# Optimization experiments

Hardware: AMD Instinct MI355X
Metric: run time of the kernel (lower is better)

## Reference

```python
import jax, jax.numpy as jnp
import numpy as np

N_NODES = 10000
N_EDGES = 640000
D = 128  # node / edge / hidden feature dim
EPS = 1e-6


def _relu_mlp(x, params):
    # Dense+relu for all layers except the last (plain Dense)
    for w, b in params[:-1]:
        x = jax.nn.relu(x @ w + b)
    w, b = params[-1]
    return x @ w + b


def _layer_norm(x, scale, bias):
    mean = jnp.mean(x, axis=-1, keepdims=True)
    var = jnp.mean(jnp.square(x - mean), axis=-1, keepdims=True)
    return (x - mean) * jax.lax.rsqrt(var + EPS) * scale + bias


def _he(key, fan_in, fan_out):
    return jax.random.normal(key, (fan_in, fan_out), jnp.float32) * jnp.sqrt(2.0 / fan_in)


def setup_inputs() -> dict:
    key = jax.random.key(0)
    ks = jax.random.split(key, 12)
    nodes = jax.random.normal(ks[0], (N_NODES, D), jnp.float32)
    edges = jax.random.normal(ks[1], (N_EDGES, D), jnp.float32)
    senders = jax.random.randint(ks[2], (N_EDGES,), 0, N_NODES, jnp.int32)
    receivers = jax.random.randint(ks[3], (N_EDGES,), 0, N_NODES, jnp.int32)
    # MessageMLP: [3D -> D -> D -> D]
    msg_w0 = _he(ks[4], 3 * D, D); msg_b0 = jnp.zeros((D,), jnp.float32)
    msg_w1 = _he(ks[5], D, D);     msg_b1 = jnp.zeros((D,), jnp.float32)
    msg_w2 = _he(ks[6], D, D);     msg_b2 = jnp.zeros((D,), jnp.float32)
    # NodeMLP: [2D -> D -> D -> D]
    node_w0 = _he(ks[7], 2 * D, D); node_b0 = jnp.zeros((D,), jnp.float32)
    node_w1 = _he(ks[8], D, D);     node_b1 = jnp.zeros((D,), jnp.float32)
    node_w2 = _he(ks[9], D, D);     node_b2 = jnp.zeros((D,), jnp.float32)
    # W_node residual projection (no bias) + LayerNorm params
    w_node = _he(ks[10], D, D)
    ln_scale = jnp.ones((D,), jnp.float32)
    ln_bias = jnp.zeros((D,), jnp.float32)
    return dict(nodes=nodes, edges=edges, senders=senders, receivers=receivers,
                msg_w0=msg_w0, msg_b0=msg_b0, msg_w1=msg_w1, msg_b1=msg_b1,
                msg_w2=msg_w2, msg_b2=msg_b2,
                node_w0=node_w0, node_b0=node_b0, node_w1=node_w1, node_b1=node_b1,
                node_w2=node_w2, node_b2=node_b2,
                w_node=w_node, ln_scale=ln_scale, ln_bias=ln_bias)


def reference(nodes, edges, senders, receivers,
              msg_w0, msg_b0, msg_w1, msg_b1, msg_w2, msg_b2,
              node_w0, node_b0, node_w1, node_b1, node_w2, node_b2,
              w_node, ln_scale, ln_bias):
    total_nodes = nodes.shape[0]
    # gather sender/receiver features and concat with edge features: [E, 3D]
    msg_in = jnp.concatenate([nodes[senders], nodes[receivers], edges], axis=-1)
    messages = _relu_mlp(msg_in, [(msg_w0, msg_b0), (msg_w1, msg_b1), (msg_w2, msg_b2)])
    # scatter-add messages onto receiving nodes: [N, D]
    aggregated = jax.ops.segment_sum(messages, receivers, num_segments=total_nodes)
    node_in = jnp.concatenate([nodes, aggregated], axis=-1)  # [N, 2D]
    nodes_out = _relu_mlp(node_in, [(node_w0, node_b0), (node_w1, node_b1), (node_w2, node_b2)])
    nodes_new = _layer_norm(nodes @ w_node + nodes_out, ln_scale, ln_bias)
    return nodes_new
```

## Files before the change

kernel.cpp:

```cpp
#include <hip/hip_runtime.h>

#define DF 128
constexpr int N_NODES = 10000;
constexpr int N_EDGES = 640000;

typedef __bf16 bf16x8 __attribute__((ext_vector_type(8)));
typedef float f32x4 __attribute__((ext_vector_type(4)));

__device__ __forceinline__ unsigned short f2bf(float f) {
  unsigned u = __builtin_bit_cast(unsigned, f);
  u += 0x7fffu + ((u >> 16) & 1u);
  return (unsigned short)(u >> 16);
}

__device__ __forceinline__ bf16x8 cvt8(float4 a, float4 b) {
  bf16x8 r;
  r[0] = (__bf16)a.x; r[1] = (__bf16)a.y; r[2] = (__bf16)a.z; r[3] = (__bf16)a.w;
  r[4] = (__bf16)b.x; r[5] = (__bf16)b.y; r[6] = (__bf16)b.z; r[7] = (__bf16)b.w;
  return r;
}

template <bool RELU>
__device__ __forceinline__ void stage_t(char* bufj, const f32x4* accv, int grp, int row16) {
#pragma unroll
  for (int nt = 0; nt < 8; ++nt)
#pragma unroll
    for (int i = 0; i < 4; ++i) {
      const int r = grp * 4 + i;
      const int c = nt * 16 + row16;
      float v = RELU ? fmaxf(accv[nt][i], 0.f) : accv[nt][i];
      *(unsigned short*)(bufj + ((r * 256 + c * 2) ^ ((r & 7) << 4))) = f2bf(v);
    }
}

__device__ __forceinline__ bf16x8 read_a(const char* bufj, int kt, int grp, int row16) {
  return *(const bf16x8*)(bufj + ((row16 * 256 + kt * 64 + grp * 16) ^ ((row16 & 7) << 4)));
}

__global__ void zero_deg(int* __restrict__ deg) {
  int i = blockIdx.x * 256 + threadIdx.x;
  if (i < N_NODES) deg[i] = 0;
}

__global__ void pack_prep(const float* __restrict__ w0, const float* __restrict__ w1,
                          const float* __restrict__ w2, const float* __restrict__ nw0,
                          const float* __restrict__ nw1, const float* __restrict__ nw2,
                          const float* __restrict__ wn, const float* __restrict__ nodes,
                          const int* __restrict__ receivers,
                          unsigned short* __restrict__ dst, unsigned short* __restrict__ nbf,
                          int* __restrict__ deg) {
  int tid = blockIdx.x * blockDim.x + threadIdx.x;
  if (tid < 163840) {
    const float* src; int p;
    if (tid < 49152)       { src = w0;  p = tid; }
    else if (tid < 65536)  { src = w1;  p = tid - 49152; }
    else if (tid < 81920)  { src = w2;  p = tid - 65536; }
    else if (tid < 114688) { src = nw0; p = tid - 81920; }
    else if (tid < 131072) { src = nw1; p = tid - 114688; }
    else if (tid < 147456) { src = nw2; p = tid - 131072; }
    else                   { src = wn;  p = tid - 147456; }
    int i = p & 7, lane = (p >> 3) & 63, tile = p >> 9;
    int nt = tile & 7, kt = tile >> 3;
    int k = kt * 32 + ((lane >> 4) << 3) + i;
    int n = nt * 16 + (lane & 15);
    dst[tid] = f2bf(src[k * 128 + n]);
    return;
  }
  int p = tid - 163840;
  if (p < N_NODES * DF) {
    nbf[p] = f2bf(nodes[p]);
    return;
  }
  p -= N_NODES * DF;
  if (p < N_EDGES) atomicAdd(&deg[receivers[p]], 1);
}

__global__ void scan_kernel(const int* __restrict__ deg, int* __restrict__ cursor) {
  __shared__ int part[1024];
  const int t = threadIdx.x;
  int loc[16];
  int s = 0;
#pragma unroll
  for (int j = 0; j < 16; ++j) {
    int idx = t * 16 + j;
    int v = (idx < N_NODES) ? deg[idx] : 0;
    loc[j] = s;
    s += v;
  }
  part[t] = s;
  __syncthreads();
  for (int off = 1; off < 1024; off <<= 1) {
    int v = part[t];
    int a = (t >= off) ? part[t - off] : 0;
    __syncthreads();
    part[t] = v + a;
    __syncthreads();
  }
  int base = (t > 0) ? part[t - 1] : 0;
#pragma unroll
  for (int j = 0; j < 16; ++j) {
    int idx = t * 16 + j;
    if (idx < N_NODES) cursor[idx] = base + loc[j];
  }
}

__global__ void __launch_bounds__(256) scatter_copy(
    const int* __restrict__ receivers, const int* __restrict__ senders,
    const float* __restrict__ edges,
    int* __restrict__ cursor, int* __restrict__ ssend, int* __restrict__ rid,
    unsigned short* __restrict__ esort,
    const unsigned short* __restrict__ nbf, const unsigned short* __restrict__ pw,
    unsigned short* __restrict__ P, unsigned short* __restrict__ Q,
    float* __restrict__ hsum) {
  __shared__ int qsh[256];
  const int bid = blockIdx.x;
  const int tid = threadIdx.x;
  if (bid < N_EDGES / 256) {
    const int e = bid * 256 + tid;
    const int r = receivers[e];
    const int q = atomicAdd(&cursor[r], 1);
    ssend[q] = senders[e];
    rid[q] = r;
    qsh[tid] = q;
    __syncthreads();
    const int sub = tid & 15;
    const int g16 = tid >> 4;
#pragma unroll
    for (int j = 0; j < 16; ++j) {
      const int i = g16 + j * 16;
      const int ee = bid * 256 + i;
      const int qq = qsh[i];
      const float* src = edges + (size_t)ee * DF + sub * 8;
      float4 a = *(const float4*)src;
      float4 b = *(const float4*)(src + 4);
      *(bf16x8*)(esort + (size_t)qq * DF + sub * 8) = cvt8(a, b);
    }
    return;
  }
  const int pb = bid - N_EDGES / 256;
  const int base_row = pb * 64;
  const int nrows = min(64, N_NODES - base_row);
  {
    float4* hz = (float4*)(hsum + (size_t)base_row * DF);
    for (int c = tid; c < nrows * 32; c += 256) hz[c] = make_float4(0.f, 0.f, 0.f, 0.f);
  }
  const int lane = tid & 63, wave = tid >> 6;
  const int row16 = lane & 15, grp = lane >> 4;
  const int rb = base_row + wave * 16;
  const int rA = min(rb + row16, N_NODES - 1);

  f32x4 aP[8], aQ[8];
#pragma unroll
  for (int nt = 0; nt < 8; ++nt) {
    aP[nt] = (f32x4){0.f, 0.f, 0.f, 0.f};
    aQ[nt] = (f32x4){0.f, 0.f, 0.f, 0.f};
  }
#pragma unroll
  for (int kt = 0; kt < 4; ++kt) {
    bf16x8 af = *(const bf16x8*)(nbf + (size_t)rA * DF + kt * 32 + grp * 8);
#pragma unroll
    for (int nt = 0; nt < 8; ++nt) {
      bf16x8 bwP = *(const bf16x8*)(pw + ((size_t)(kt * 8 + nt) * 64 + lane) * 8);
      bf16x8 bwQ = *(const bf16x8*)(pw + ((size_t)((4 + kt) * 8 + nt) * 64 + lane) * 8);
      aP[nt] = __builtin_amdgcn_mfma_f32_16x16x32_bf16(af, bwP, aP[nt], 0, 0, 0);
      aQ[nt] = __builtin_amdgcn_mfma_f32_16x16x32_bf16(af, bwQ, aQ[nt], 0, 0, 0);
    }
  }
#pragma unroll
  for (int nt = 0; nt < 8; ++nt)
#pragma unroll
    for (int i = 0; i < 4; ++i) {
      const int r = rb + grp * 4 + i;
      if (r < N_NODES) {
        P[(size_t)r * DF + nt * 16 + row16] = f2bf(aP[nt][i]);
        Q[(size_t)r * DF + nt * 16 + row16] = f2bf(aQ[nt][i]);
      }
    }
}

__global__ void __launch_bounds__(512, 2) msg_kernel(
    const unsigned short* __restrict__ esort,
    const int* __restrict__ ssend, const int* __restrict__ rid,
    const float* __restrict__ b0, const float* __restrict__ b1,
    const unsigned short* __restrict__ pw,
    const unsigned short* __restrict__ P, const unsigned short* __restrict__ Q,
    float* __restrict__ hsum) {
  __shared__ char lds[131072];
  const int tid = threadIdx.x;
  const int lane = tid & 63, wave = tid >> 6;
  const int row16 = lane & 15, grp = lane >> 4;
  char* hb = lds + 65536 + wave * 8192;

  {
    const float4* src = (const float4*)(pw + 32768);
    float4* dst = (float4*)lds;
    for (int c = tid; c < 4096; c += 512) dst[c] = src[c];
  }

  constexpr int NTILE = N_EDGES / 256;
  int tile = blockIdx.x;

  bf16x8 ebf_c[2][4], ebf_n[2][4];
  int sxc[2], rxc[2], sx2[2], rx2[2];

  {
    const int pb = tile * 256 + wave * 32;
#pragma unroll
    for (int s = 0; s < 2; ++s) {
      sxc[s] = ssend[pb + s * 16 + row16];
      rxc[s] = rid[pb + s * 16 + row16];
#pragma unroll
      for (int kt = 0; kt < 4; ++kt)
        ebf_c[s][kt] = *(const bf16x8*)(esort + (size_t)(pb + s * 16 + row16) * DF +
                                        kt * 32 + grp * 8);
    }
  }

  __syncthreads();

  for (; tile < NTILE; tile += 256) {
    const int pbase = tile * 256 + wave * 32;
    const bool hasNext = (tile + 256) < NTILE;

    if (hasNext) {
      const int npb = (tile + 256) * 256 + wave * 32;
#pragma unroll
      for (int s = 0; s < 2; ++s) {
        sx2[s] = ssend[npb + s * 16 + row16];
        rx2[s] = rid[npb + s * 16 + row16];
#pragma unroll
        for (int kt = 0; kt < 4; ++kt)
          ebf_n[s][kt] = *(const bf16x8*)(esort + (size_t)(npb + s * 16 + row16) * DF +
                                          kt * 32 + grp * 8);
      }
    }

    bf16x8 pqf[2][2][4];
#pragma unroll
    for (int s = 0; s < 2; ++s)
#pragma unroll
      for (int kt = 0; kt < 4; ++kt) {
        pqf[s][0][kt] = *(const bf16x8*)(P + (size_t)sxc[s] * DF + kt * 32 + grp * 8);
        pqf[s][1][kt] = *(const bf16x8*)(Q + (size_t)rxc[s] * DF + kt * 32 + grp * 8);
      }

    f32x4 acc[2][8];
#pragma unroll
    for (int nt = 0; nt < 8; ++nt) {
      float bv = b0[nt * 16 + row16];
      acc[0][nt] = (f32x4){bv, bv, bv, bv};
      acc[1][nt] = (f32x4){bv, bv, bv, bv};
    }
#pragma unroll
    for (int kt = 0; kt < 4; ++kt) {
#pragma unroll
      for (int nt = 0; nt < 8; ++nt) {
        bf16x8 bw = *(const bf16x8*)(lds + ((kt * 8 + nt) * 64 + lane) * 16);
        acc[0][nt] = __builtin_amdgcn_mfma_f32_16x16x32_bf16(ebf_c[0][kt], bw, acc[0][nt], 0, 0, 0);
        acc[1][nt] = __builtin_amdgcn_mfma_f32_16x16x32_bf16(ebf_c[1][kt], bw, acc[1][nt], 0, 0, 0);
      }
    }

    stage_t<false>(hb, acc[0], grp, row16);
    stage_t<false>(hb + 4096, acc[1], grp, row16);
    asm volatile("s_waitcnt lgkmcnt(0)" ::: "memory");
    __builtin_amdgcn_sched_barrier(0);

#pragma unroll
    for (int nt = 0; nt < 8; ++nt) {
      float bv = b1[nt * 16 + row16];
      acc[0][nt] = (f32x4){bv, bv, bv, bv};
      acc[1][nt] = (f32x4){bv, bv, bv, bv};
    }
#pragma unroll
    for (int kt = 0; kt < 4; ++kt) {
      bf16x8 af[2];
#pragma unroll
      for (int s = 0; s < 2; ++s) {
        bf16x8 raw = read_a(hb + s * 4096, kt, grp, row16);
        bf16x8 pv = pqf[s][0][kt], qv = pqf[s][1][kt];
        bf16x8 h;
#pragma unroll
        for (int j = 0; j < 8; ++j)
          h[j] = (__bf16)fmaxf((float)raw[j] + (float)pv[j] + (float)qv[j], 0.f);
        af[s] = h;
      }
#pragma unroll
      for (int nt = 0; nt < 8; ++nt) {
        bf16x8 bw = *(const bf16x8*)(lds + 32768 + ((kt * 8 + nt) * 64 + lane) * 16);
        acc[0][nt] = __builtin_amdgcn_mfma_f32_16x16x32_bf16(af[0], bw, acc[0][nt], 0, 0, 0);
        acc[1][nt] = __builtin_amdgcn_mfma_f32_16x16x32_bf16(af[1], bw, acc[1][nt], 0, 0, 0);
      }
    }

#pragma unroll
    for (int s = 0; s < 2; ++s) {
      const int q = pbase + s * 16 + grp * 4;
      const int ru = rid[pbase + s * 16];
      const bool uni = (ru == rid[pbase + s * 16 + 15]);
      if (uni) {
#pragma unroll
        for (int nt = 0; nt < 8; ++nt) {
          float t = fmaxf(acc[s][nt][0], 0.f) + fmaxf(acc[s][nt][1], 0.f) +
                    fmaxf(acc[s][nt][2], 0.f) + fmaxf(acc[s][nt][3], 0.f);
          t += __shfl_xor(t, 16);
          t += __shfl_xor(t, 32);
          if (grp == 0)
            unsafeAtomicAdd(hsum + (size_t)ru * DF + nt * 16 + row16, t);
        }
      } else {
        const int ra = rid[q], rb_ = rid[q + 1], rc = rid[q + 2], rd = rid[q + 3];
#pragma unroll
        for (int nt = 0; nt < 8; ++nt) {
          const int col = nt * 16 + row16;
          float run = fmaxf(acc[s][nt][0], 0.f);
          if (rb_ != ra) { unsafeAtomicAdd(hsum + (size_t)ra * DF + col, run); run = 0.f; }
          run += fmaxf(acc[s][nt][1], 0.f);
          if (rc != rb_) { unsafeAtomicAdd(hsum + (size_t)rb_ * DF + col, run); run = 0.f; }
          run += fmaxf(acc[s][nt][2], 0.f);
          if (rd != rc) { unsafeAtomicAdd(hsum + (size_t)rc * DF + col, run); run = 0.f; }
          run += fmaxf(acc[s][nt][3], 0.f);
          unsafeAtomicAdd(hsum + (size_t)rd * DF + col, run);
        }
      }
    }

#pragma unroll
    for (int s = 0; s < 2; ++s) {
      sxc[s] = sx2[s]; rxc[s] = rx2[s];
#pragma unroll
      for (int kt = 0; kt < 4; ++kt) ebf_c[s][kt] = ebf_n[s][kt];
    }
    asm volatile("s_waitcnt lgkmcnt(0)" ::: "memory");
    __builtin_amdgcn_sched_barrier(0);
  }
}

__global__ void __launch_bounds__(128) node_kernel(
    const float* __restrict__ nodes, const float* __restrict__ hsum,
    const int* __restrict__ deg, const float* __restrict__ b2,
    const float* __restrict__ nb0, const float* __restrict__ nb1, const float* __restrict__ nb2,
    const unsigned short* __restrict__ pw2,
    const unsigned short* __restrict__ pnw0, const unsigned short* __restrict__ pnw1,
    const unsigned short* __restrict__ pnw2, const unsigned short* __restrict__ pwn,
    const float* __restrict__ ln_s, const float* __restrict__ ln_b,
    float* __restrict__ out) {
  __shared__ char hs[8192];
  const int tid = threadIdx.x, lane = tid & 63, wave = tid >> 6;
  const int row16 = lane & 15, grp = lane >> 4;
  char* hb = hs + wave * 4096;
  const int rb = blockIdx.x * 32 + wave * 16;
  const int rA = min(rb + row16, N_NODES - 1);

  f32x4 accA[8];
  {
    float d0 = (float)deg[min(rb + grp * 4 + 0, N_NODES - 1)];
    float d1 = (float)deg[min(rb + grp * 4 + 1, N_NODES - 1)];
    float d2 = (float)deg[min(rb + grp * 4 + 2, N_NODES - 1)];
    float d3 = (float)deg[min(rb + grp * 4 + 3, N_NODES - 1)];
#pragma unroll
    for (int nt = 0; nt < 8; ++nt) {
      float bc = b2[nt * 16 + row16];
      accA[nt] = (f32x4){d0 * bc, d1 * bc, d2 * bc, d3 * bc};
    }
  }
#pragma unroll
  for (int kt = 0; kt < 4; ++kt) {
    const float* hp = hsum + (size_t)rA * DF + kt * 32 + grp * 8;
    float4 h0 = *(const float4*)hp, h1v = *(const float4*)(hp + 4);
    bf16x8 hi = cvt8(h0, h1v);
    float4 l0, l1;
    l0.x = h0.x - (float)hi[0]; l0.y = h0.y - (float)hi[1];
    l0.z = h0.z - (float)hi[2]; l0.w = h0.w - (float)hi[3];
    l1.x = h1v.x - (float)hi[4]; l1.y = h1v.y - (float)hi[5];
    l1.z = h1v.z - (float)hi[6]; l1.w = h1v.w - (float)hi[7];
    bf16x8 lo = cvt8(l0, l1);
#pragma unroll
    for (int nt = 0; nt < 8; ++nt) {
      bf16x8 bw = *(const bf16x8*)(pw2 + ((size_t)(kt * 8 + nt) * 64 + lane) * 8);
      accA[nt] = __builtin_amdgcn_mfma_f32_16x16x32_bf16(hi, bw, accA[nt], 0, 0, 0);
      accA[nt] = __builtin_amdgcn_mfma_f32_16x16x32_bf16(lo, bw, accA[nt], 0, 0, 0);
    }
  }
  stage_t<false>(hb, accA, grp, row16);
  asm volatile("s_waitcnt lgkmcnt(0)" ::: "memory");
  __builtin_amdgcn_sched_barrier(0);

  f32x4 acc[8];
#pragma unroll
  for (int nt = 0; nt < 8; ++nt) {
    float b = nb0[nt * 16 + row16];
    acc[nt] = (f32x4){b, b, b, b};
  }
#pragma unroll
  for (int kt = 0; kt < 8; ++kt) {
    bf16x8 af;
    if (kt < 4) {
      const float* p = nodes + (size_t)rA * DF + kt * 32 + grp * 8;
      af = cvt8(*(const float4*)p, *(const float4*)(p + 4));
    } else {
      af = read_a(hb, kt - 4, grp, row16);
    }
#pragma unroll
    for (int nt = 0; nt < 8; ++nt) {
      bf16x8 bw = *(const bf16x8*)(pnw0 + ((size_t)(kt * 8 + nt) * 64 + lane) * 8);
      acc[nt] = __builtin_amdgcn_mfma_f32_16x16x32_bf16(af, bw, acc[nt], 0, 0, 0);
    }
  }
  asm volatile("s_waitcnt lgkmcnt(0)" ::: "memory");
  __builtin_amdgcn_sched_barrier(0);
  stage_t<true>(hb, acc, grp, row16);
  asm volatile("s_waitcnt lgkmcnt(0)" ::: "memory");
  __builtin_amdgcn_sched_barrier(0);

  f32x4 acc2[8];
#pragma unroll
  for (int nt = 0; nt < 8; ++nt) {
    float b = nb1[nt * 16 + row16];
    acc2[nt] = (f32x4){b, b, b, b};
  }
#pragma unroll
  for (int kt = 0; kt < 4; ++kt) {
    bf16x8 af = read_a(hb, kt, grp, row16);
#pragma unroll
    for (int nt = 0; nt < 8; ++nt) {
      bf16x8 bw = *(const bf16x8*)(pnw1 + ((size_t)(kt * 8 + nt) * 64 + lane) * 8);
      acc2[nt] = __builtin_amdgcn_mfma_f32_16x16x32_bf16(af, bw, acc2[nt], 0, 0, 0);
    }
  }
  asm volatile("s_waitcnt lgkmcnt(0)" ::: "memory");
  __builtin_amdgcn_sched_barrier(0);
  stage_t<true>(hb, acc2, grp, row16);
  asm volatile("s_waitcnt lgkmcnt(0)" ::: "memory");
  __builtin_amdgcn_sched_barrier(0);

  f32x4 acc3[8];
#pragma unroll
  for (int nt = 0; nt < 8; ++nt) {
    float b = nb2[nt * 16 + row16];
    acc3[nt] = (f32x4){b, b, b, b};
  }
#pragma unroll
  for (int kt = 0; kt < 4; ++kt) {
    bf16x8 af = read_a(hb, kt, grp, row16);
#pragma unroll
    for (int nt = 0; nt < 8; ++nt) {
      bf16x8 bw = *(const bf16x8*)(pnw2 + ((size_t)(kt * 8 + nt) * 64 + lane) * 8);
      acc3[nt] = __builtin_amdgcn_mfma_f32_16x16x32_bf16(af, bw, acc3[nt], 0, 0, 0);
    }
  }
  f32x4 accR[8];
#pragma unroll
  for (int nt = 0; nt < 8; ++nt) accR[nt] = (f32x4){0.f, 0.f, 0.f, 0.f};
#pragma unroll
  for (int kt = 0; kt < 4; ++kt) {
    const float* p = nodes + (size_t)rA * DF + kt * 32 + grp * 8;
    bf16x8 af = cvt8(*(const float4*)p, *(const float4*)(p + 4));
#pragma unroll
    for (int nt = 0; nt < 8; ++nt) {
      bf16x8 bw = *(const bf16x8*)(pwn + ((size_t)(kt * 8 + nt) * 64 + lane) * 8);
      accR[nt] = __builtin_amdgcn_mfma_f32_16x16x32_bf16(af, bw, accR[nt], 0, 0, 0);
    }
  }

  float y[8][4];
#pragma unroll
  for (int nt = 0; nt < 8; ++nt)
#pragma unroll
    for (int i = 0; i < 4; ++i) y[nt][i] = acc3[nt][i] + accR[nt][i];

  float mean[4], rstd[4];
#pragma unroll
  for (int i = 0; i < 4; ++i) {
    float s = 0.f;
#pragma unroll
    for (int nt = 0; nt < 8; ++nt) s += y[nt][i];
    s += __shfl_xor(s, 1); s += __shfl_xor(s, 2);
    s += __shfl_xor(s, 4); s += __shfl_xor(s, 8);
    mean[i] = s * (1.0f / 128.0f);
  }
#pragma unroll
  for (int i = 0; i < 4; ++i) {
    float v = 0.f;
#pragma unroll
    for (int nt = 0; nt < 8; ++nt) {
      float d = y[nt][i] - mean[i];
      v += d * d;
    }
    v += __shfl_xor(v, 1); v += __shfl_xor(v, 2);
    v += __shfl_xor(v, 4); v += __shfl_xor(v, 8);
    rstd[i] = rsqrtf(v * (1.0f / 128.0f) + 1e-6f);
  }
#pragma unroll
  for (int nt = 0; nt < 8; ++nt) {
    const float ls = ln_s[nt * 16 + row16];
    const float lb = ln_b[nt * 16 + row16];
#pragma unroll
    for (int i = 0; i < 4; ++i) {
      const int r = rb + grp * 4 + i;
      if (r < N_NODES)
        out[(size_t)r * DF + nt * 16 + row16] = (y[nt][i] - mean[i]) * rstd[i] * ls + lb;
    }
  }
}

extern "C" void kernel_launch(void* const* d_in, const int* in_sizes, int n_in,
                              void* d_out, int out_size, void* d_ws, size_t ws_size,
                              hipStream_t stream) {
  const float* nodes     = (const float*)d_in[0];
  const float* edges     = (const float*)d_in[1];
  const int*   senders   = (const int*)d_in[2];
  const int*   receivers = (const int*)d_in[3];
  const float* msg_w0 = (const float*)d_in[4];
  const float* msg_b0 = (const float*)d_in[5];
  const float* msg_w1 = (const float*)d_in[6];
  const float* msg_b1 = (const float*)d_in[7];
  const float* msg_w2 = (const float*)d_in[8];
  const float* msg_b2 = (const float*)d_in[9];
  const float* node_w0 = (const float*)d_in[10];
  const float* node_b0 = (const float*)d_in[11];
  const float* node_w1 = (const float*)d_in[12];
  const float* node_b1 = (const float*)d_in[13];
  const float* node_w2 = (const float*)d_in[14];
  const float* node_b2 = (const float*)d_in[15];
  const float* w_node   = (const float*)d_in[16];
  const float* ln_scale = (const float*)d_in[17];
  const float* ln_bias  = (const float*)d_in[18];

  char* ws = (char*)d_ws;
  float* hsum           = (float*)ws;
  unsigned short* pw    = (unsigned short*)(ws + 5120000);
  unsigned short* nbf   = (unsigned short*)(ws + 5447680);
  int* deg              = (int*)(ws + 8007680);
  int* cursor           = (int*)(ws + 8047680);
  int* rid              = (int*)(ws + 8087680);
  int* ssend            = (int*)(ws + 10647680);
  unsigned short* P     = (unsigned short*)(ws + 13207680);
  unsigned short* Q     = (unsigned short*)(ws + 15767680);
  unsigned short* esort = (unsigned short*)(ws + 18327680);

  zero_deg<<<40, 256, 0, stream>>>(deg);

  pack_prep<<<8140, 256, 0, stream>>>(
      msg_w0, msg_w1, msg_w2, node_w0, node_w1, node_w2, w_node, nodes, receivers,
      pw, nbf, deg);

  scan_kernel<<<1, 1024, 0, stream>>>(deg, cursor);

  scatter_copy<<<N_EDGES / 256 + 157, 256, 0, stream>>>(
      receivers, senders, edges, cursor, ssend, rid, esort, nbf, pw, P, Q, hsum);

  msg_kernel<<<256, 512, 0, stream>>>(
      esort, ssend, rid, msg_b0, msg_b1, pw, P, Q, hsum);

  node_kernel<<<313, 128, 0, stream>>>(nodes, hsum, deg, msg_b2,
                                       node_b0, node_b1, node_b2,
                                       pw + 65536,
                                       pw + 81920, pw + 114688, pw + 131072, pw + 147456,
                                       ln_scale, ln_bias, (float*)d_out);
}
```

Measured before the change: 342.4 us.

## Move edge-part of first message layer into scatter kernel before sorting

The edge-feature slice of the first message MLP layer (edges @ W0c + b0) is now computed in the scatter kernel with MFMA, right after the edges are read, and the bf16 result is scattered into receiver-sorted order instead of the raw edge features. The message kernel then loads these precomputed partial activations directly into registers, which drops one GEMM, an LDS staging round trip and the first-layer weights from LDS, so LDS use falls from 128KB to 32KB. In exchange the scatter kernel reads the weights from global memory per wave, needs 32KB of LDS for the transpose staging, and rounds the layer-0 partial sum to bf16 before P and Q are added.

```diff
diff --git a/kernel.cpp b/kernel.cpp
--- a/kernel.cpp
+++ b/kernel.cpp
@@ -104,15 +104,16 @@
   }
 }
 
-__global__ void __launch_bounds__(256) scatter_copy(
+__global__ void __launch_bounds__(256) scatter_l0(
     const int* __restrict__ receivers, const int* __restrict__ senders,
-    const float* __restrict__ edges,
+    const float* __restrict__ edges, const float* __restrict__ b0,
     int* __restrict__ cursor, int* __restrict__ ssend, int* __restrict__ rid,
-    unsigned short* __restrict__ esort,
+    unsigned short* __restrict__ rsort,
     const unsigned short* __restrict__ nbf, const unsigned short* __restrict__ pw,
     unsigned short* __restrict__ P, unsigned short* __restrict__ Q,
     float* __restrict__ hsum) {
   __shared__ int qsh[256];
+  __shared__ char tbuf[32768];
   const int bid = blockIdx.x;
   const int tid = threadIdx.x;
   if (bid < N_EDGES / 256) {
@@ -123,17 +124,57 @@
     rid[q] = r;
     qsh[tid] = q;
     __syncthreads();
-    const int sub = tid & 15;
-    const int g16 = tid >> 4;
-#pragma unroll
-    for (int j = 0; j < 16; ++j) {
-      const int i = g16 + j * 16;
-      const int ee = bid * 256 + i;
-      const int qq = qsh[i];
-      const float* src = edges + (size_t)ee * DF + sub * 8;
-      float4 a = *(const float4*)src;
-      float4 b = *(const float4*)(src + 4);
-      *(bf16x8*)(esort + (size_t)qq * DF + sub * 8) = cvt8(a, b);
+    const int lane = tid & 63, wave = tid >> 6;
+    const int row16 = lane & 15, grp = lane >> 4;
+    char* tb = tbuf + wave * 8192;
+    const unsigned short* w0c = pw + 32768;
+#pragma unroll
+    for (int pass = 0; pass < 2; ++pass) {
+      bf16x8 ebf[2][4];
+#pragma unroll
+      for (int s = 0; s < 2; ++s) {
+        const int eloc = bid * 256 + wave * 64 + (pass * 2 + s) * 16 + row16;
+#pragma unroll
+        for (int kt = 0; kt < 4; ++kt) {
+          const float* p = edges + (size_t)eloc * DF + kt * 32 + grp * 8;
+          ebf[s][kt] = cvt8(*(const float4*)p, *(const float4*)(p + 4));
+        }
+      }
+      f32x4 acc[2][8];
+#pragma unroll
+      for (int nt = 0; nt < 8; ++nt) {
+        float bv = b0[nt * 16 + row16];
+        acc[0][nt] = (f32x4){bv, bv, bv, bv};
+        acc[1][nt] = (f32x4){bv, bv, bv, bv};
+      }
+#pragma unroll
+      for (int kt = 0; kt < 4; ++kt) {
+#pragma unroll
+        for (int nt = 0; nt < 8; ++nt) {
+          bf16x8 bw = *(const bf16x8*)(w0c + ((size_t)(kt * 8 + nt) * 64 + lane) * 8);
+          acc[0][nt] = __builtin_amdgcn_mfma_f32_16x16x32_bf16(ebf[0][kt], bw, acc[0][nt], 0, 0, 0);
+          acc[1][nt] = __builtin_amdgcn_mfma_f32_16x16x32_bf16(ebf[1][kt], bw, acc[1][nt], 0, 0, 0);
+        }
+      }
+      stage_t<false>(tb, acc[0], grp, row16);
+      stage_t<false>(tb + 4096, acc[1], grp, row16);
+      asm volatile("s_waitcnt lgkmcnt(0)" ::: "memory");
+      __builtin_amdgcn_sched_barrier(0);
+#pragma unroll
+      for (int s = 0; s < 2; ++s) {
+#pragma unroll
+        for (int j = 0; j < 4; ++j) {
+          const int idx = j * 64 + lane;
+          const int row = idx >> 4;
+          const int chunk = idx & 15;
+          const int qq = qsh[wave * 64 + (pass * 2 + s) * 16 + row];
+          bf16x8 v = *(const bf16x8*)(tb + s * 4096 +
+                                      ((row * 256 + chunk * 16) ^ ((row & 7) << 4)));
+          *(bf16x8*)(rsort + (size_t)qq * DF + chunk * 8) = v;
+        }
+      }
+      asm volatile("s_waitcnt lgkmcnt(0)" ::: "memory");
+      __builtin_amdgcn_sched_barrier(0);
     }
     return;
   }
@@ -179,40 +220,39 @@
 }
 
 __global__ void __launch_bounds__(512, 2) msg_kernel(
-    const unsigned short* __restrict__ esort,
+    const unsigned short* __restrict__ rsort,
     const int* __restrict__ ssend, const int* __restrict__ rid,
-    const float* __restrict__ b0, const float* __restrict__ b1,
+    const float* __restrict__ b1,
     const unsigned short* __restrict__ pw,
     const unsigned short* __restrict__ P, const unsigned short* __restrict__ Q,
     float* __restrict__ hsum) {
-  __shared__ char lds[131072];
+  __shared__ char lds[32768];
   const int tid = threadIdx.x;
   const int lane = tid & 63, wave = tid >> 6;
   const int row16 = lane & 15, grp = lane >> 4;
-  char* hb = lds + 65536 + wave * 8192;
 
   {
-    const float4* src = (const float4*)(pw + 32768);
+    const float4* src = (const float4*)(pw + 49152);
     float4* dst = (float4*)lds;
-    for (int c = tid; c < 4096; c += 512) dst[c] = src[c];
+    for (int c = tid; c < 2048; c += 512) dst[c] = src[c];
   }
 
   constexpr int NTILE = N_EDGES / 256;
   int tile = blockIdx.x;
 
-  bf16x8 ebf_c[2][4], ebf_n[2][4];
+  bf16x8 raw_c[2][4], raw_n[2][4];
   int sxc[2], rxc[2], sx2[2], rx2[2];
 
   {
     const int pb = tile * 256 + wave * 32;
 #pragma unroll
     for (int s = 0; s < 2; ++s) {
-      sxc[s] = ssend[pb + s * 16 + row16];
-      rxc[s] = rid[pb + s * 16 + row16];
+      const int pos = pb + s * 16 + row16;
+      sxc[s] = ssend[pos];
+      rxc[s] = rid[pos];
 #pragma unroll
       for (int kt = 0; kt < 4; ++kt)
-        ebf_c[s][kt] = *(const bf16x8*)(esort + (size_t)(pb + s * 16 + row16) * DF +
-                                        kt * 32 + grp * 8);
+        raw_c[s][kt] = *(const bf16x8*)(rsort + (size_t)pos * DF + kt * 32 + grp * 8);
     }
   }
 
@@ -226,12 +266,12 @@
       const int npb = (tile + 256) * 256 + wave * 32;
 #pragma unroll
       for (int s = 0; s < 2; ++s) {
-        sx2[s] = ssend[npb + s * 16 + row16];
-        rx2[s] = rid[npb + s * 16 + row16];
+        const int pos = npb + s * 16 + row16;
+        sx2[s] = ssend[pos];
+        rx2[s] = rid[pos];
 #pragma unroll
         for (int kt = 0; kt < 4; ++kt)
-          ebf_n[s][kt] = *(const bf16x8*)(esort + (size_t)(npb + s * 16 + row16) * DF +
-                                          kt * 32 + grp * 8);
+          raw_n[s][kt] = *(const bf16x8*)(rsort + (size_t)pos * DF + kt * 32 + grp * 8);
       }
     }
 
@@ -247,27 +287,6 @@
     f32x4 acc[2][8];
 #pragma unroll
     for (int nt = 0; nt < 8; ++nt) {
-      float bv = b0[nt * 16 + row16];
-      acc[0][nt] = (f32x4){bv, bv, bv, bv};
-      acc[1][nt] = (f32x4){bv, bv, bv, bv};
-    }
-#pragma unroll
-    for (int kt = 0; kt < 4; ++kt) {
-#pragma unroll
-      for (int nt = 0; nt < 8; ++nt) {
-        bf16x8 bw = *(const bf16x8*)(lds + ((kt * 8 + nt) * 64 + lane) * 16);
-        acc[0][nt] = __builtin_amdgcn_mfma_f32_16x16x32_bf16(ebf_c[0][kt], bw, acc[0][nt], 0, 0, 0);
-        acc[1][nt] = __builtin_amdgcn_mfma_f32_16x16x32_bf16(ebf_c[1][kt], bw, acc[1][nt], 0, 0, 0);
-      }
-    }
-
-    stage_t<false>(hb, acc[0], grp, row16);
-    stage_t<false>(hb + 4096, acc[1], grp, row16);
-    asm volatile("s_waitcnt lgkmcnt(0)" ::: "memory");
-    __builtin_amdgcn_sched_barrier(0);
-
-#pragma unroll
-    for (int nt = 0; nt < 8; ++nt) {
       float bv = b1[nt * 16 + row16];
       acc[0][nt] = (f32x4){bv, bv, bv, bv};
       acc[1][nt] = (f32x4){bv, bv, bv, bv};
@@ -277,7 +296,7 @@
       bf16x8 af[2];
 #pragma unroll
       for (int s = 0; s < 2; ++s) {
-        bf16x8 raw = read_a(hb + s * 4096, kt, grp, row16);
+        bf16x8 raw = raw_c[s][kt];
         bf16x8 pv = pqf[s][0][kt], qv = pqf[s][1][kt];
         bf16x8 h;
 #pragma unroll
@@ -287,7 +306,7 @@
       }
 #pragma unroll
       for (int nt = 0; nt < 8; ++nt) {
-        bf16x8 bw = *(const bf16x8*)(lds + 32768 + ((kt * 8 + nt) * 64 + lane) * 16);
+        bf16x8 bw = *(const bf16x8*)(lds + ((kt * 8 + nt) * 64 + lane) * 16);
         acc[0][nt] = __builtin_amdgcn_mfma_f32_16x16x32_bf16(af[0], bw, acc[0][nt], 0, 0, 0);
         acc[1][nt] = __builtin_amdgcn_mfma_f32_16x16x32_bf16(af[1], bw, acc[1][nt], 0, 0, 0);
       }
@@ -329,10 +348,8 @@
     for (int s = 0; s < 2; ++s) {
       sxc[s] = sx2[s]; rxc[s] = rx2[s];
 #pragma unroll
-      for (int kt = 0; kt < 4; ++kt) ebf_c[s][kt] = ebf_n[s][kt];
-    }
-    asm volatile("s_waitcnt lgkmcnt(0)" ::: "memory");
-    __builtin_amdgcn_sched_barrier(0);
+      for (int kt = 0; kt < 4; ++kt) raw_c[s][kt] = raw_n[s][kt];
+    }
   }
 }
 
@@ -537,7 +554,7 @@
   int* ssend            = (int*)(ws + 10647680);
   unsigned short* P     = (unsigned short*)(ws + 13207680);
   unsigned short* Q     = (unsigned short*)(ws + 15767680);
-  unsigned short* esort = (unsigned short*)(ws + 18327680);
+  unsigned short* rsort = (unsigned short*)(ws + 18327680);
 
   zero_deg<<<40, 256, 0, stream>>>(deg);
 
@@ -547,11 +564,11 @@
 
   scan_kernel<<<1, 1024, 0, stream>>>(deg, cursor);
 
-  scatter_copy<<<N_EDGES / 256 + 157, 256, 0, stream>>>(
-      receivers, senders, edges, cursor, ssend, rid, esort, nbf, pw, P, Q, hsum);
+  scatter_l0<<<N_EDGES / 256 + 157, 256, 0, stream>>>(
+      receivers, senders, edges, msg_b0, cursor, ssend, rid, rsort, nbf, pw, P, Q, hsum);
 
   msg_kernel<<<256, 512, 0, stream>>>(
-      esort, ssend, rid, msg_b0, msg_b1, pw, P, Q, hsum);
+      rsort, ssend, rid, msg_b1, pw, P, Q, hsum);
 
   node_kernel<<<313, 128, 0, stream>>>(nodes, hsum, deg, msg_b2,
                                        node_b0, node_b1, node_b2,
```

Measured after the change: 542.1 us. +58.3%, slower.
